# Kernel tuning notes

Measured on AMD Instinct MI355X. Metric: run time of the kernel, lower is better.

Reference implementation:

```python
import jax, jax.numpy as jnp
import numpy as np
from functools import partial

D = 256        # encoder_output_size
F = 256        # duration_predictor_filter_size
K = 3          # kernel size, padding=1
EPS = 1e-5
ALPHA = 1.0


def _xavier(key, shape, fan_in, fan_out, gain):
    a = gain * np.sqrt(6.0 / (fan_in + fan_out))
    return jax.random.uniform(key, shape, jnp.float32, -a, a)


def setup_inputs() -> dict:
    key = jax.random.key(0)
    ks = jax.random.split(key, 8)
    B, S = 32, 1024
    relu_gain = float(np.sqrt(2.0))
    inp = {
        "encoder_output": jax.random.normal(ks[0], (B, S, D), jnp.float32),
        "encoder_output_mask": jnp.ones((B, S, 1), jnp.float32),
        "target": jax.random.randint(ks[1], (B, S), 0, 3, jnp.int64),
        "mel_max_length": 4096,
        # conv weights in WIO layout [K, in, out]
        "W1": _xavier(ks[2], (K, D, F), D * K, F * K, relu_gain),
        "b1": jnp.zeros((F,), jnp.float32),
        "g1": jnp.ones((F,), jnp.float32),
        "beta1": jnp.zeros((F,), jnp.float32),
        "W2": _xavier(ks[3], (K, F, F), F * K, F * K, relu_gain),
        "b2": jnp.zeros((F,), jnp.float32),
        "g2": jnp.ones((F,), jnp.float32),
        "beta2": jnp.zeros((F,), jnp.float32),
        "Wl": _xavier(ks[4], (F, 1), F, 1, relu_gain),
        "bl": jnp.zeros((1,), jnp.float32),
    }
    return inp


def _conv1d(x, W, b):
    # x: [B,S,C], W: [K,Cin,Cout], padding=1 (same for K=3)
    y = jax.lax.conv_general_dilated(
        x, W, window_strides=(1,), padding=[(1, 1)],
        dimension_numbers=("NWC", "WIO", "NWC"))
    return y + b


def _layer_norm(x, g, b):
    mu = jnp.mean(x, axis=-1, keepdims=True)
    var = jnp.mean(jnp.square(x - mu), axis=-1, keepdims=True)
    return (x - mu) * jax.lax.rsqrt(var + EPS) * g + b


def _duration_predictor(x, mask, W1, b1, g1, beta1, W2, b2, g2, beta2, Wl, bl):
    x = x * mask
    h = jax.nn.relu(_layer_norm(_conv1d(x, W1, b1), g1, beta1))
    h = jax.nn.relu(_layer_norm(_conv1d(h, W2, b2), g2, beta2))
    d = jnp.einsum("bsf,fo->bso", h, Wl) + bl            # [B,S,1]
    d = jax.nn.relu(d * mask[:, :, 0:1])
    return d[..., 0]                                      # [B,S]


def _length_regulate(enc, target, alpha, mel_max_length):
    B, S, _ = enc.shape
    Tmax = mel_max_length
    # round-half-up as in the original rounding(), then +1 (source expands dur+1 times)
    reps = jnp.floor(target.astype(jnp.float32) * alpha + 0.5).astype(jnp.int32) + 1
    cum = jnp.cumsum(reps, axis=1)                        # [B,S]
    t = jnp.arange(Tmax, dtype=jnp.int32)                 # [Tmax]
    idx = jax.vmap(lambda c: jnp.searchsorted(c, t, side="right"))(cum)  # [B,Tmax]
    valid = t[None, :] < cum[:, -1:]                      # [B,Tmax]
    idx = jnp.minimum(idx, S - 1)
    out = jnp.take_along_axis(enc, idx[..., None], axis=1) * valid[..., None].astype(enc.dtype)
    pos = jnp.where(valid, t[None, :] + 1, 0).astype(jnp.int64)
    return out, pos


def reference(encoder_output, encoder_output_mask, target, mel_max_length,
              W1, b1, g1, beta1, W2, b2, g2, beta2, Wl, bl):
    dur_pred = _duration_predictor(encoder_output, encoder_output_mask,
                                   W1, b1, g1, beta1, W2, b2, g2, beta2, Wl, bl)
    output, decoder_pos = _length_regulate(encoder_output, target, ALPHA, mel_max_length)
    return output, decoder_pos, dur_pred
```

## Files before the change

### kernel.cpp

```cpp
#include <hip/hip_runtime.h>
#include <hip/hip_bf16.h>

#define BATCH 32
#define SEQ   1024
#define DCH   256
#define TMAX  4096
#define MROWS (BATCH * SEQ)
#define EPS   1e-5f

typedef __attribute__((ext_vector_type(8))) short s16x8;
typedef __attribute__((ext_vector_type(4))) float f32x4;

#define NSTEPS 24
#define WP_SHORTS (NSTEPS * 8192)

#define XROWS      68
#define H1_OFF     4096
#define H1_STRIDE  528
#define P_STRIDE   136
#define HP_STRIDE  68
#define ST_OFF     38944
#define LDS_TOTAL  39472

#define CONV_BLOCKS 512
#define REG_BLOCKS  2048
#define GRID_TOTAL  (CONV_BLOCKS + REG_BLOCKS)

__device__ __forceinline__ short f2bf_t(float f) {
    union { float f; unsigned u; } x; x.f = f;
    return (short)(x.u >> 16);
}
__device__ __forceinline__ short f2bf(float f) {
    union { float f; unsigned u; } x; x.f = f;
    unsigned r = x.u + 0x7fffu + ((x.u >> 16) & 1u);
    return (short)(r >> 16);
}
__device__ __forceinline__ unsigned pack_bf2(float lo, float hi) {
    union { float f; unsigned u; } a, b; a.f = lo; b.f = hi;
    return (a.u >> 16) | (b.u & 0xffff0000u);
}

__global__ __launch_bounds__(256) void prep_kernel(
    const float* __restrict__ W1, const float* __restrict__ W2,
    short* __restrict__ Wp1, short* __restrict__ Wp2,
    const int* __restrict__ target, int* __restrict__ idx,
    float* __restrict__ out_pos)
{
    const int bx  = blockIdx.x;
    const int tid = threadIdx.x;
    if (bx < 48) {
        const int s = bx % NSTEPS;
        const float* W = (bx < NSTEPS) ? W1 : W2;
        short* out = (bx < NSTEPS) ? Wp1 : Wp2;
        const int n  = tid;
        const int wv = n >> 6;
        const int nc = (n >> 4) & 3;
        const int cl = n & 15;
        const int ko = s >> 3;
        const int cb = (s & 7) * 32;
        #pragma unroll
        for (int q = 0; q < 4; ++q) {
            short v[8];
            #pragma unroll
            for (int j = 0; j < 8; ++j)
                v[j] = f2bf(W[(size_t)(ko * 256 + cb + q * 8 + j) * 256 + n]);
            short* dst = out + s * 8192 + wv * 2048 + nc * 512 + (q * 16 + cl) * 8;
            *(s16x8*)dst = *(const s16x8*)v;
        }
    } else {
        const int b = bx - 48;
        const int base = tid * 4;
        int reps[4], vals[4];
        int s = 0;
        #pragma unroll
        for (int j = 0; j < 4; ++j) {
            reps[j] = target[b * SEQ + base + j] + 1;
            s += reps[j];
            vals[j] = s;
        }
        const int lane = tid & 63;
        int tot = s;
        #pragma unroll
        for (int off = 1; off < 64; off <<= 1) {
            int t = __shfl_up(tot, off, 64);
            if (lane >= off) tot += t;
        }
        __shared__ int wsum[4];
        const int wid = tid >> 6;
        if (lane == 63) wsum[wid] = tot;
        __syncthreads();
        int woff = 0;
        for (int w = 0; w < wid; ++w) woff += wsum[w];
        const int total = wsum[0] + wsum[1] + wsum[2] + wsum[3];
        const int thr_excl = tot - s + woff;
        int* ib = idx + b * TMAX;
        #pragma unroll
        for (int j = 0; j < 4; ++j) {
            const int end   = thr_excl + vals[j];
            const int start = end - reps[j];
            for (int t = start; t < end; ++t) ib[t] = base + j;
        }
        for (int t = total + tid; t < TMAX; t += 256) ib[t] = -1;
        float* pb_ = out_pos + b * TMAX;
        for (int t = tid; t < TMAX; t += 256)
            pb_[t] = (t < total) ? (float)(t + 1) : 0.f;
    }
}

__global__ __launch_bounds__(256, 3) void fused_kernel(
    const float* __restrict__ enc,
    const float* __restrict__ mask,
    const short* __restrict__ Wp1,
    const short* __restrict__ Wp2,
    const float* __restrict__ cb1, const float* __restrict__ g1, const float* __restrict__ be1,
    const float* __restrict__ cb2, const float* __restrict__ g2, const float* __restrict__ be2,
    const float* __restrict__ Wl, const float* __restrict__ bl,
    float* __restrict__ out_dur,
    const int*  __restrict__ idx,
    float* __restrict__ out_main)
{
    __shared__ __align__(16) char lds[LDS_TOTAL];
    const int tid = threadIdx.x;
    const int bx  = blockIdx.x;

    if (bx >= CONV_BLOCKS) {
        const int r  = bx - CONV_BLOCKS;
        const int b  = r >> 6;
        const int t0 = (r & 63) * 64;
        int* sidx = (int*)lds;
        if (tid < 64) sidx[tid] = idx[b * TMAX + t0 + tid];
        __syncthreads();
        const int f4 = (tid & 63) * 4;
        const int rg = tid >> 6;
        #pragma unroll
        for (int g = 0; g < 16; ++g) {
            const int tt = g * 4 + rg;
            const int si = sidx[tt];
            float4 v = make_float4(0.f, 0.f, 0.f, 0.f);
            if (si >= 0)
                v = *reinterpret_cast<const float4*>(enc + (size_t)(b * SEQ + si) * 256 + f4);
            *reinterpret_cast<float4*>(out_main + (size_t)(b * TMAX + t0 + tt) * 256 + f4) = v;
        }
        return;
    }

    char* const Xst = lds;

    const int lane = tid & 63;
    const int wv   = tid >> 6;
    const int cl   = lane & 15;
    const int q    = lane >> 4;
    const int m0   = bx * 64;
    const int blo  = m0 & ~(SEQ - 1);
    const int bhi  = blo + SEQ;

    for (int t = tid; t < XROWS * 32; t += 256) {
        const int r  = t >> 5;
        const int ch = t & 31;
        const int grow = m0 - 2 + r;
        s16x8 v = {0, 0, 0, 0, 0, 0, 0, 0};
        if (grow >= blo && grow < bhi) {
            const float* xf = enc + (size_t)grow * DCH + ch * 8;
            const float4 f0 = *(const float4*)xf;
            const float4 f1 = *(const float4*)(xf + 4);
            const float mk = mask[grow];
            v[0] = f2bf_t(f0.x * mk); v[1] = f2bf_t(f0.y * mk);
            v[2] = f2bf_t(f0.z * mk); v[3] = f2bf_t(f0.w * mk);
            v[4] = f2bf_t(f1.x * mk); v[5] = f2bf_t(f1.y * mk);
            v[6] = f2bf_t(f1.z * mk); v[7] = f2bf_t(f1.w * mk);
        }
        *(s16x8*)(Xst + r * 512 + ((ch ^ (r & 7)) << 4)) = v;
    }

    f32x4 acc1[5][4];
    #pragma unroll
    for (int nc = 0; nc < 4; ++nc) {
        const f32x4 b4 = *(const f32x4*)(cb1 + wv * 64 + nc * 16 + q * 4);
        #pragma unroll
        for (int mr = 0; mr < 5; ++mr) acc1[mr][nc] = b4;
    }

    const short* wb1 = Wp1 + wv * 2048 + lane * 8;
    const short* wb2 = Wp2 + wv * 2048 + lane * 8;

#define G1_STEP(P, S)                                                         \
    {                                                                         \
        const int ko_  = (S) >> 3;                                            \
        const int chb_ = ((S) & 7) * 4 + q;                                   \
        _Pragma("unroll")                                                     \
        for (int mr = 0; mr < 5; ++mr) {                                      \
            int tr = mr * 16 + cl + ko_;                                      \
            if (mr == 4) tr = (tr < XROWS - 1) ? tr : (XROWS - 1);            \
            const s16x8 a = *(const s16x8*)(Xst + tr * 512 +                  \
                                            ((chb_ ^ (tr & 7)) << 4));        \
            _Pragma("unroll")                                                 \
            for (int nc = 0; nc < 4; ++nc)                                    \
                acc1[mr][nc] = __builtin_amdgcn_mfma_f32_16x16x32_bf16(       \
                    P[nc], a, acc1[mr][nc], 0, 0, 0);                         \
        }                                                                     \
    }
#define G2_STEP(P, S)                                                         \
    {                                                                         \
        const int ko_  = (S) >> 3;                                            \
        const int chb_ = ((S) & 7) * 4 + q;                                   \
        _Pragma("unroll")                                                     \
        for (int mr = 0; mr < 4; ++mr) {                                      \
            const int tr = mr * 16 + cl + ko_;                                \
            const s16x8 a = *(const s16x8*)(lds + H1_OFF + tr * H1_STRIDE +   \
                                            chb_ * 16);                       \
            _Pragma("unroll")                                                 \
            for (int nc = 0; nc < 4; ++nc)                                    \
                acc2[mr][nc] = __builtin_amdgcn_mfma_f32_16x16x32_bf16(       \
                    P[nc], a, acc2[mr][nc], 0, 0, 0);                         \
        }                                                                     \
    }
#define RELOAD(P, WB, S)                                                      \
    {                                                                         \
        const short* w_ = (WB) + (S) * 8192;                                  \
        _Pragma("unroll")                                                     \
        for (int nc = 0; nc < 4; ++nc)                                        \
            P[nc] = *(const s16x8*)(w_ + nc * 512);                           \
    }

    s16x8 pa[4], pb[4], pc[4];
    RELOAD(pa, wb1, 0)
    RELOAD(pb, wb1, 1)
    RELOAD(pc, wb1, 2)

    __syncthreads();

    for (int it = 0; it < 7; ++it) {
        const int s = it * 3;
        G1_STEP(pa, s)     RELOAD(pa, wb1, s + 3)
        G1_STEP(pb, s + 1) RELOAD(pb, wb1, s + 4)
        G1_STEP(pc, s + 2) RELOAD(pc, wb1, s + 5)
    }
    G1_STEP(pa, 21)
    G1_STEP(pb, 22)
    G1_STEP(pc, 23)

    float* st1 = (float*)(lds + ST_OFF);
    __syncthreads();
    #pragma unroll
    for (int mr = 0; mr < 5; ++mr) {
        float s1 = 0.f, s2 = 0.f;
        #pragma unroll
        for (int nc = 0; nc < 4; ++nc)
            #pragma unroll
            for (int rg = 0; rg < 4; ++rg) {
                const float v = acc1[mr][nc][rg];
                s1 += v; s2 += v * v;
            }
        const int hr = mr * 16 + cl;
        if (hr < 66)
            *(float2*)(lds + hr * P_STRIDE + (wv * 4 + q) * 8) = make_float2(s1, s2);
    }
    __syncthreads();
    if (tid < 66) {
        float s1 = 0.f, s2 = 0.f;
        #pragma unroll
        for (int k = 0; k < 16; ++k) {
            const int sl = (tid + k) & 15;
            const float2 v = *(const float2*)(lds + tid * P_STRIDE + sl * 8);
            s1 += v.x; s2 += v.y;
        }
        const float mean = s1 * (1.f / 256.f);
        const float var  = s2 * (1.f / 256.f) - mean * mean;
        st1[tid * 2]     = mean;
        st1[tid * 2 + 1] = rsqrtf(var + EPS);
    }
    __syncthreads();

    {
        #pragma unroll
        for (int mr = 0; mr < 5; ++mr) {
            const int hr = mr * 16 + cl;
            if (hr < 66) {
                const int grow = m0 - 1 + hr;
                const bool inb = (grow >= blo) && (grow < bhi);
                const float2 ms = *(const float2*)(st1 + hr * 2);
                #pragma unroll
                for (int nc = 0; nc < 4; ++nc) {
                    const int ch0 = wv * 64 + nc * 16 + q * 4;
                    const f32x4 g4 = *(const f32x4*)(g1 + ch0);
                    const f32x4 b4 = *(const f32x4*)(be1 + ch0);
                    float v[4];
                    #pragma unroll
                    for (int rg = 0; rg < 4; ++rg) {
                        float x = (acc1[mr][nc][rg] - ms.x) * ms.y * g4[rg] + b4[rg];
                        v[rg] = inb ? fmaxf(x, 0.f) : 0.f;
                    }
                    uint2 w;
                    w.x = pack_bf2(v[0], v[1]);
                    w.y = pack_bf2(v[2], v[3]);
                    *(uint2*)(lds + H1_OFF + hr * H1_STRIDE + ch0 * 2) = w;
                }
            }
        }
    }
    f32x4 acc2[4][4];
    RELOAD(pa, wb2, 0)
    RELOAD(pb, wb2, 1)
    RELOAD(pc, wb2, 2)
    #pragma unroll
    for (int nc = 0; nc < 4; ++nc) {
        const f32x4 b4 = *(const f32x4*)(cb2 + wv * 64 + nc * 16 + q * 4);
        #pragma unroll
        for (int mr = 0; mr < 4; ++mr) acc2[mr][nc] = b4;
    }
    __syncthreads();

    for (int it = 0; it < 7; ++it) {
        const int s = it * 3;
        G2_STEP(pa, s)     RELOAD(pa, wb2, s + 3)
        G2_STEP(pb, s + 1) RELOAD(pb, wb2, s + 4)
        G2_STEP(pc, s + 2) RELOAD(pc, wb2, s + 5)
    }
    G2_STEP(pa, 21)
    G2_STEP(pb, 22)
    G2_STEP(pc, 23)

    float* st2 = (float*)(lds + ST_OFF);
    __syncthreads();
    #pragma unroll
    for (int mr = 0; mr < 4; ++mr) {
        float s1 = 0.f, s2 = 0.f;
        #pragma unroll
        for (int nc = 0; nc < 4; ++nc)
            #pragma unroll
            for (int rg = 0; rg < 4; ++rg) {
                const float v = acc2[mr][nc][rg];
                s1 += v; s2 += v * v;
            }
        const int r = mr * 16 + cl;
        *(float2*)(lds + r * P_STRIDE + (wv * 4 + q) * 8) = make_float2(s1, s2);
    }
    __syncthreads();
    if (tid < 64) {
        float s1 = 0.f, s2 = 0.f;
        #pragma unroll
        for (int k = 0; k < 16; ++k) {
            const int sl = (tid + k) & 15;
            const float2 v = *(const float2*)(lds + tid * P_STRIDE + sl * 8);
            s1 += v.x; s2 += v.y;
        }
        const float mean = s1 * (1.f / 256.f);
        const float var  = s2 * (1.f / 256.f) - mean * mean;
        st2[tid * 2]     = mean;
        st2[tid * 2 + 1] = rsqrtf(var + EPS);
    }
    __syncthreads();

    {
        #pragma unroll
        for (int mr = 0; mr < 4; ++mr) {
            const int r = mr * 16 + cl;
            const float2 ms = *(const float2*)(st2 + r * 2);
            float p = 0.f;
            #pragma unroll
            for (int nc = 0; nc < 4; ++nc) {
                const int ch0 = wv * 64 + nc * 16 + q * 4;
                const f32x4 g4 = *(const f32x4*)(g2 + ch0);
                const f32x4 b4 = *(const f32x4*)(be2 + ch0);
                const f32x4 w4 = *(const f32x4*)(Wl + ch0);
                #pragma unroll
                for (int rg = 0; rg < 4; ++rg) {
                    float x = (acc2[mr][nc][rg] - ms.x) * ms.y * g4[rg] + b4[rg];
                    p += fmaxf(x, 0.f) * w4[rg];
                }
            }
            *(float*)(lds + r * HP_STRIDE + (wv * 4 + q) * 4) = p;
        }
        __syncthreads();
        if (tid < 64) {
            float d = 0.f;
            #pragma unroll
            for (int k = 0; k < 16; ++k) {
                const int sl = (tid + k) & 15;
                d += *(const float*)(lds + tid * HP_STRIDE + sl * 4);
            }
            d += bl[0];
            d *= mask[m0 + tid];
            out_dur[m0 + tid] = fmaxf(d, 0.f);
        }
    }
}

extern "C" void kernel_launch(void* const* d_in, const int* in_sizes, int n_in,
                              void* d_out, int out_size, void* d_ws, size_t ws_size,
                              hipStream_t stream) {
    const float* enc   = (const float*)d_in[0];
    const float* mask  = (const float*)d_in[1];
    const int*   target= (const int*)  d_in[2];
    const float* W1    = (const float*)d_in[4];
    const float* b1    = (const float*)d_in[5];
    const float* g1    = (const float*)d_in[6];
    const float* beta1 = (const float*)d_in[7];
    const float* W2    = (const float*)d_in[8];
    const float* b2    = (const float*)d_in[9];
    const float* g2    = (const float*)d_in[10];
    const float* beta2 = (const float*)d_in[11];
    const float* Wl    = (const float*)d_in[12];
    const float* bl    = (const float*)d_in[13];

    float* outF = (float*)d_out;
    float* out_main = outF;
    float* out_pos  = outF + (size_t)BATCH * TMAX * DCH;
    float* out_dur  = out_pos + (size_t)BATCH * TMAX;

    char* ws = (char*)d_ws;
    short* Wp1 = (short*)ws;
    short* Wp2 = Wp1 + WP_SHORTS;
    int*   idx = (int*)(Wp2 + WP_SHORTS);

    prep_kernel<<<80, 256, 0, stream>>>(W1, W2, Wp1, Wp2, target, idx, out_pos);
    fused_kernel<<<GRID_TOTAL, 256, 0, stream>>>(
        enc, mask, Wp1, Wp2,
        b1, g1, beta1, b2, g2, beta2, Wl, bl,
        out_dur, idx, out_main);
}
```

Measured before the change: 58.72 us.

## Split conv1 into two row passes and reuse input LDS for hidden activations

Conv1 accumulators are split into two passes (3 then 2 row tiles) so fewer accumulator registers are live at once, and the weight prefetch drops from triple to double buffering. The conv1 pre-norm output is stored as bf16 in place of the input tile, then LayerNorm+ReLU runs over LDS in a separate pass, which removes the separate H1 buffer and shrinks LDS. Cross-lane partial sums now use shuffles instead of 16-way LDS reductions. The cost is recomputing the weight stream twice for conv1, an extra LDS pass, and LN statistics taken from fp32 but applied to bf16-rounded values.

```diff
diff --git a/kernel.cpp b/kernel.cpp
--- a/kernel.cpp
+++ b/kernel.cpp
@@ -15,12 +15,9 @@
 #define WP_SHORTS (NSTEPS * 8192)
 
 #define XROWS      68
-#define H1_OFF     4096
-#define H1_STRIDE  528
-#define P_STRIDE   136
-#define HP_STRIDE  68
-#define ST_OFF     38944
-#define LDS_TOTAL  39472
+#define ST_OFF     34816
+#define PART_OFF   35344
+#define LDS_TOTAL  37984
 
 #define CONV_BLOCKS 512
 #define REG_BLOCKS  2048
@@ -38,6 +35,11 @@
 __device__ __forceinline__ unsigned pack_bf2(float lo, float hi) {
     union { float f; unsigned u; } a, b; a.f = lo; b.f = hi;
     return (a.u >> 16) | (b.u & 0xffff0000u);
+}
+__device__ __forceinline__ float bf2f(short s) {
+    union { unsigned u; float f; } x;
+    x.u = ((unsigned)(unsigned short)s) << 16;
+    return x.f;
 }
 
 __global__ __launch_bounds__(256) void prep_kernel(
@@ -107,6 +109,14 @@
     }
 }
 
+#define RELOAD(P, WB, S)                                                      \
+    {                                                                         \
+        const short* w_ = (WB) + (S) * 8192;                                  \
+        _Pragma("unroll")                                                     \
+        for (int nc = 0; nc < 4; ++nc)                                        \
+            P[nc] = *(const s16x8*)(w_ + nc * 512);                           \
+    }
+
 __global__ __launch_bounds__(256, 3) void fused_kernel(
     const float* __restrict__ enc,
     const float* __restrict__ mask,
@@ -172,158 +182,217 @@
         *(s16x8*)(Xst + r * 512 + ((ch ^ (r & 7)) << 4)) = v;
     }
 
-    f32x4 acc1[5][4];
+    const short* wb1 = Wp1 + wv * 2048 + lane * 8;
+    const short* wb2 = Wp2 + wv * 2048 + lane * 8;
+    float* st1 = (float*)(lds + ST_OFF);
+
+    s16x8 p0[4], p1[4];
+    RELOAD(p0, wb1, 0)
+    RELOAD(p1, wb1, 1)
+
+    f32x4 accA[3][4];
     #pragma unroll
     for (int nc = 0; nc < 4; ++nc) {
         const f32x4 b4 = *(const f32x4*)(cb1 + wv * 64 + nc * 16 + q * 4);
         #pragma unroll
-        for (int mr = 0; mr < 5; ++mr) acc1[mr][nc] = b4;
-    }
-
-    const short* wb1 = Wp1 + wv * 2048 + lane * 8;
-    const short* wb2 = Wp2 + wv * 2048 + lane * 8;
-
-#define G1_STEP(P, S)                                                         \
+        for (int mr = 0; mr < 3; ++mr) accA[mr][nc] = b4;
+    }
+    __syncthreads();
+
+#define GA_STEP(P, S)                                                         \
     {                                                                         \
         const int ko_  = (S) >> 3;                                            \
         const int chb_ = ((S) & 7) * 4 + q;                                   \
         _Pragma("unroll")                                                     \
-        for (int mr = 0; mr < 5; ++mr) {                                      \
-            int tr = mr * 16 + cl + ko_;                                      \
-            if (mr == 4) tr = (tr < XROWS - 1) ? tr : (XROWS - 1);            \
+        for (int mr = 0; mr < 3; ++mr) {                                      \
+            const int tr = mr * 16 + cl + ko_;                     \
             const s16x8 a = *(const s16x8*)(Xst + tr * 512 +                  \
                                             ((chb_ ^ (tr & 7)) << 4));        \
             _Pragma("unroll")                                                 \
             for (int nc = 0; nc < 4; ++nc)                                    \
-                acc1[mr][nc] = __builtin_amdgcn_mfma_f32_16x16x32_bf16(       \
-                    P[nc], a, acc1[mr][nc], 0, 0, 0);                         \
+                accA[mr][nc] = __builtin_amdgcn_mfma_f32_16x16x32_bf16(       \
+                    P[nc], a, accA[mr][nc], 0, 0, 0);                         \
         }                                                                     \
     }
+    for (int s = 0; s < NSTEPS; s += 2) {
+        GA_STEP(p0, s)
+        if (s + 2 < NSTEPS) RELOAD(p0, wb1, s + 2)
+        GA_STEP(p1, s + 1)
+        if (s + 3 < NSTEPS) RELOAD(p1, wb1, s + 3)
+    }
+
+    __syncthreads();
+
+    #pragma unroll
+    for (int mr = 0; mr < 3; ++mr) {
+        const int hr = mr * 16 + cl;
+        float s1 = 0.f, s2 = 0.f;
+        #pragma unroll
+        for (int nc = 0; nc < 4; ++nc)
+            #pragma unroll
+            for (int rg = 0; rg < 4; ++rg) {
+                const float v = accA[mr][nc][rg];
+                s1 += v; s2 += v * v;
+            }
+        s1 += __shfl_xor(s1, 16, 64); s1 += __shfl_xor(s1, 32, 64);
+        s2 += __shfl_xor(s2, 16, 64); s2 += __shfl_xor(s2, 32, 64);
+        if (lane < 16)
+            *(float2*)(lds + PART_OFF + hr * 40 + wv * 8) = make_float2(s1, s2);
+        #pragma unroll
+        for (int nc = 0; nc < 4; ++nc) {
+            const int ch0 = wv * 64 + nc * 16 + q * 4;
+            const int c16 = ch0 >> 3;
+            uint2 w;
+            w.x = pack_bf2(accA[mr][nc][0], accA[mr][nc][1]);
+            w.y = pack_bf2(accA[mr][nc][2], accA[mr][nc][3]);
+            *(uint2*)(lds + hr * 512 + ((c16 ^ (hr & 7)) << 4) + (q & 1) * 8) = w;
+        }
+    }
+
+    RELOAD(p0, wb1, 0)
+    RELOAD(p1, wb1, 1)
+    f32x4 accB[2][4];
+    #pragma unroll
+    for (int nc = 0; nc < 4; ++nc) {
+        const f32x4 b4 = *(const f32x4*)(cb1 + wv * 64 + nc * 16 + q * 4);
+        #pragma unroll
+        for (int mr = 0; mr < 2; ++mr) accB[mr][nc] = b4;
+    }
+#define GB_STEP(P, S)                                                         \
+    {                                                                         \
+        const int ko_  = (S) >> 3;                                            \
+        const int chb_ = ((S) & 7) * 4 + q;                                   \
+        _Pragma("unroll")                                                     \
+        for (int mr = 0; mr < 2; ++mr) {                                      \
+            int tr = 48 + mr * 16 + cl + ko_;                                 \
+            if (mr == 1) tr = (tr < XROWS - 1) ? tr : (XROWS - 1);            \
+            const s16x8 a = *(const s16x8*)(Xst + tr * 512 +                  \
+                                            ((chb_ ^ (tr & 7)) << 4));        \
+            _Pragma("unroll")                                                 \
+            for (int nc = 0; nc < 4; ++nc)                                    \
+                accB[mr][nc] = __builtin_amdgcn_mfma_f32_16x16x32_bf16(       \
+                    P[nc], a, accB[mr][nc], 0, 0, 0);                         \
+        }                                                                     \
+    }
+    for (int s = 0; s < NSTEPS; s += 2) {
+        GB_STEP(p0, s)
+        if (s + 2 < NSTEPS) RELOAD(p0, wb1, s + 2)
+        GB_STEP(p1, s + 1)
+        if (s + 3 < NSTEPS) RELOAD(p1, wb1, s + 3)
+    }
+
+    __syncthreads();
+
+    #pragma unroll
+    for (int mr = 0; mr < 2; ++mr) {
+        const int hr = 48 + mr * 16 + cl;
+        float s1 = 0.f, s2 = 0.f;
+        #pragma unroll
+        for (int nc = 0; nc < 4; ++nc)
+            #pragma unroll
+            for (int rg = 0; rg < 4; ++rg) {
+                const float v = accB[mr][nc][rg];
+                s1 += v; s2 += v * v;
+            }
+        s1 += __shfl_xor(s1, 16, 64); s1 += __shfl_xor(s1, 32, 64);
+        s2 += __shfl_xor(s2, 16, 64); s2 += __shfl_xor(s2, 32, 64);
+        if (hr < 66) {
+            if (lane < 16)
+                *(float2*)(lds + PART_OFF + hr * 40 + wv * 8) = make_float2(s1, s2);
+            #pragma unroll
+            for (int nc = 0; nc < 4; ++nc) {
+                const int ch0 = wv * 64 + nc * 16 + q * 4;
+                const int c16 = ch0 >> 3;
+                uint2 w;
+                w.x = pack_bf2(accB[mr][nc][0], accB[mr][nc][1]);
+                w.y = pack_bf2(accB[mr][nc][2], accB[mr][nc][3]);
+                *(uint2*)(lds + hr * 512 + ((c16 ^ (hr & 7)) << 4) + (q & 1) * 8) = w;
+            }
+        }
+    }
+
+    RELOAD(p0, wb2, 0)
+    RELOAD(p1, wb2, 1)
+
+    __syncthreads();
+
+    if (tid < 66) {
+        const char* pb = lds + PART_OFF + tid * 40;
+        const float2 a0 = *(const float2*)pb;
+        const float2 a1 = *(const float2*)(pb + 8);
+        const float2 a2 = *(const float2*)(pb + 16);
+        const float2 a3 = *(const float2*)(pb + 24);
+        const float s1 = a0.x + a1.x + a2.x + a3.x;
+        const float s2 = a0.y + a1.y + a2.y + a3.y;
+        const float mean = s1 * (1.f / 256.f);
+        const float var  = s2 * (1.f / 256.f) - mean * mean;
+        st1[tid * 2]     = mean;
+        st1[tid * 2 + 1] = rsqrtf(var + EPS);
+    }
+    __syncthreads();
+
+    for (int i = tid; i < 66 * 32; i += 256) {
+        const int r   = i >> 5;
+        const int c16 = i & 31;
+        char* p = lds + r * 512 + ((c16 ^ (r & 7)) << 4);
+        const int grow = m0 - 1 + r;
+        if (grow >= blo && grow < bhi) {
+            const float2 ms = *(const float2*)(st1 + r * 2);
+            const f32x4 gA = *(const f32x4*)(g1 + c16 * 8);
+            const f32x4 gB = *(const f32x4*)(g1 + c16 * 8 + 4);
+            const f32x4 bA = *(const f32x4*)(be1 + c16 * 8);
+            const f32x4 bB = *(const f32x4*)(be1 + c16 * 8 + 4);
+            s16x8 v = *(s16x8*)p;
+            s16x8 o;
+            #pragma unroll
+            for (int j = 0; j < 8; ++j) {
+                const float x  = bf2f(v[j]);
+                const float gg = (j < 4) ? gA[j] : gB[j - 4];
+                const float bb = (j < 4) ? bA[j] : bB[j - 4];
+                const float y  = (x - ms.x) * ms.y * gg + bb;
+                o[j] = f2bf_t(fmaxf(y, 0.f));
+            }
+            *(s16x8*)p = o;
+        } else {
+            s16x8 z = {0, 0, 0, 0, 0, 0, 0, 0};
+            *(s16x8*)p = z;
+        }
+    }
+
+    f32x4 acc2[4][4];
+    #pragma unroll
+    for (int nc = 0; nc < 4; ++nc) {
+        const f32x4 b4 = *(const f32x4*)(cb2 + wv * 64 + nc * 16 + q * 4);
+        #pragma unroll
+        for (int mr = 0; mr < 4; ++mr) acc2[mr][nc] = b4;
+    }
+    __syncthreads();
+
 #define G2_STEP(P, S)                                                         \
     {                                                                         \
         const int ko_  = (S) >> 3;                                            \
         const int chb_ = ((S) & 7) * 4 + q;                                   \
         _Pragma("unroll")                                                     \
         for (int mr = 0; mr < 4; ++mr) {                                      \
-            const int tr = mr * 16 + cl + ko_;                                \
-            const s16x8 a = *(const s16x8*)(lds + H1_OFF + tr * H1_STRIDE +   \
-                                            chb_ * 16);                       \
+            const int tr = mr * 16 + cl + ko_;                     \
+            const s16x8 a = *(const s16x8*)(Xst + tr * 512 +                  \
+                                            ((chb_ ^ (tr & 7)) << 4));        \
             _Pragma("unroll")                                                 \
             for (int nc = 0; nc < 4; ++nc)                                    \
                 acc2[mr][nc] = __builtin_amdgcn_mfma_f32_16x16x32_bf16(       \
                     P[nc], a, acc2[mr][nc], 0, 0, 0);                         \
         }                                                                     \
     }
-#define RELOAD(P, WB, S)                                                      \
-    {                                                                         \
-        const short* w_ = (WB) + (S) * 8192;                                  \
-        _Pragma("unroll")                                                     \
-        for (int nc = 0; nc < 4; ++nc)                                        \
-            P[nc] = *(const s16x8*)(w_ + nc * 512);                           \
-    }
-
-    s16x8 pa[4], pb[4], pc[4];
-    RELOAD(pa, wb1, 0)
-    RELOAD(pb, wb1, 1)
-    RELOAD(pc, wb1, 2)
-
-    __syncthreads();
-
-    for (int it = 0; it < 7; ++it) {
-        const int s = it * 3;
-        G1_STEP(pa, s)     RELOAD(pa, wb1, s + 3)
-        G1_STEP(pb, s + 1) RELOAD(pb, wb1, s + 4)
-        G1_STEP(pc, s + 2) RELOAD(pc, wb1, s + 5)
-    }
-    G1_STEP(pa, 21)
-    G1_STEP(pb, 22)
-    G1_STEP(pc, 23)
-
-    float* st1 = (float*)(lds + ST_OFF);
-    __syncthreads();
-    #pragma unroll
-    for (int mr = 0; mr < 5; ++mr) {
-        float s1 = 0.f, s2 = 0.f;
-        #pragma unroll
-        for (int nc = 0; nc < 4; ++nc)
-            #pragma unroll
-            for (int rg = 0; rg < 4; ++rg) {
-                const float v = acc1[mr][nc][rg];
-                s1 += v; s2 += v * v;
-            }
-        const int hr = mr * 16 + cl;
-        if (hr < 66)
-            *(float2*)(lds + hr * P_STRIDE + (wv * 4 + q) * 8) = make_float2(s1, s2);
-    }
-    __syncthreads();
-    if (tid < 66) {
-        float s1 = 0.f, s2 = 0.f;
-        #pragma unroll
-        for (int k = 0; k < 16; ++k) {
-            const int sl = (tid + k) & 15;
-            const float2 v = *(const float2*)(lds + tid * P_STRIDE + sl * 8);
-            s1 += v.x; s2 += v.y;
-        }
-        const float mean = s1 * (1.f / 256.f);
-        const float var  = s2 * (1.f / 256.f) - mean * mean;
-        st1[tid * 2]     = mean;
-        st1[tid * 2 + 1] = rsqrtf(var + EPS);
-    }
-    __syncthreads();
-
-    {
-        #pragma unroll
-        for (int mr = 0; mr < 5; ++mr) {
-            const int hr = mr * 16 + cl;
-            if (hr < 66) {
-                const int grow = m0 - 1 + hr;
-                const bool inb = (grow >= blo) && (grow < bhi);
-                const float2 ms = *(const float2*)(st1 + hr * 2);
-                #pragma unroll
-                for (int nc = 0; nc < 4; ++nc) {
-                    const int ch0 = wv * 64 + nc * 16 + q * 4;
-                    const f32x4 g4 = *(const f32x4*)(g1 + ch0);
-                    const f32x4 b4 = *(const f32x4*)(be1 + ch0);
-                    float v[4];
-                    #pragma unroll
-                    for (int rg = 0; rg < 4; ++rg) {
-                        float x = (acc1[mr][nc][rg] - ms.x) * ms.y * g4[rg] + b4[rg];
-                        v[rg] = inb ? fmaxf(x, 0.f) : 0.f;
-                    }
-                    uint2 w;
-                    w.x = pack_bf2(v[0], v[1]);
-                    w.y = pack_bf2(v[2], v[3]);
-                    *(uint2*)(lds + H1_OFF + hr * H1_STRIDE + ch0 * 2) = w;
-                }
-            }
-        }
-    }
-    f32x4 acc2[4][4];
-    RELOAD(pa, wb2, 0)
-    RELOAD(pb, wb2, 1)
-    RELOAD(pc, wb2, 2)
-    #pragma unroll
-    for (int nc = 0; nc < 4; ++nc) {
-        const f32x4 b4 = *(const f32x4*)(cb2 + wv * 64 + nc * 16 + q * 4);
-        #pragma unroll
-        for (int mr = 0; mr < 4; ++mr) acc2[mr][nc] = b4;
-    }
-    __syncthreads();
-
-    for (int it = 0; it < 7; ++it) {
-        const int s = it * 3;
-        G2_STEP(pa, s)     RELOAD(pa, wb2, s + 3)
-        G2_STEP(pb, s + 1) RELOAD(pb, wb2, s + 4)
-        G2_STEP(pc, s + 2) RELOAD(pc, wb2, s + 5)
-    }
-    G2_STEP(pa, 21)
-    G2_STEP(pb, 22)
-    G2_STEP(pc, 23)
-
-    float* st2 = (float*)(lds + ST_OFF);
-    __syncthreads();
+    for (int s = 0; s < NSTEPS; s += 2) {
+        G2_STEP(p0, s)
+        if (s + 2 < NSTEPS) RELOAD(p0, wb2, s + 2)
+        G2_STEP(p1, s + 1)
+        if (s + 3 < NSTEPS) RELOAD(p1, wb2, s + 3)
+    }
+
     #pragma unroll
     for (int mr = 0; mr < 4; ++mr) {
+        const int r = mr * 16 + cl;
         float s1 = 0.f, s2 = 0.f;
         #pragma unroll
         for (int nc = 0; nc < 4; ++nc)
@@ -332,18 +401,21 @@
                 const float v = acc2[mr][nc][rg];
                 s1 += v; s2 += v * v;
             }
-        const int r = mr * 16 + cl;
-        *(float2*)(lds + r * P_STRIDE + (wv * 4 + q) * 8) = make_float2(s1, s2);
-    }
-    __syncthreads();
+        s1 += __shfl_xor(s1, 16, 64); s1 += __shfl_xor(s1, 32, 64);
+        s2 += __shfl_xor(s2, 16, 64); s2 += __shfl_xor(s2, 32, 64);
+        if (lane < 16)
+            *(float2*)(lds + PART_OFF + r * 40 + wv * 8) = make_float2(s1, s2);
+    }
+    __syncthreads();
+    float* st2 = st1;
     if (tid < 64) {
-        float s1 = 0.f, s2 = 0.f;
-        #pragma unroll
-        for (int k = 0; k < 16; ++k) {
-            const int sl = (tid + k) & 15;
-            const float2 v = *(const float2*)(lds + tid * P_STRIDE + sl * 8);
-            s1 += v.x; s2 += v.y;
-        }
+        const char* pb = lds + PART_OFF + tid * 40;
+        const float2 a0 = *(const float2*)pb;
+        const float2 a1 = *(const float2*)(pb + 8);
+        const float2 a2 = *(const float2*)(pb + 16);
+        const float2 a3 = *(const float2*)(pb + 24);
+        const float s1 = a0.x + a1.x + a2.x + a3.x;
+        const float s2 = a0.y + a1.y + a2.y + a3.y;
         const float mean = s1 * (1.f / 256.f);
         const float var  = s2 * (1.f / 256.f) - mean * mean;
         st2[tid * 2]     = mean;
@@ -351,38 +423,33 @@
     }
     __syncthreads();
 
-    {
-        #pragma unroll
-        for (int mr = 0; mr < 4; ++mr) {
-            const int r = mr * 16 + cl;
-            const float2 ms = *(const float2*)(st2 + r * 2);
-            float p = 0.f;
-            #pragma unroll
-            for (int nc = 0; nc < 4; ++nc) {
-                const int ch0 = wv * 64 + nc * 16 + q * 4;
-                const f32x4 g4 = *(const f32x4*)(g2 + ch0);
-                const f32x4 b4 = *(const f32x4*)(be2 + ch0);
-                const f32x4 w4 = *(const f32x4*)(Wl + ch0);
-                #pragma unroll
-                for (int rg = 0; rg < 4; ++rg) {
-                    float x = (acc2[mr][nc][rg] - ms.x) * ms.y * g4[rg] + b4[rg];
-                    p += fmaxf(x, 0.f) * w4[rg];
-                }
-            }
-            *(float*)(lds + r * HP_STRIDE + (wv * 4 + q) * 4) = p;
-        }
-        __syncthreads();
-        if (tid < 64) {
-            float d = 0.f;
-            #pragma unroll
-            for (int k = 0; k < 16; ++k) {
-                const int sl = (tid + k) & 15;
-                d += *(const float*)(lds + tid * HP_STRIDE + sl * 4);
-            }
-            d += bl[0];
-            d *= mask[m0 + tid];
-            out_dur[m0 + tid] = fmaxf(d, 0.f);
-        }
+    #pragma unroll
+    for (int mr = 0; mr < 4; ++mr) {
+        const int r = mr * 16 + cl;
+        const float2 ms = *(const float2*)(st2 + r * 2);
+        float p = 0.f;
+        #pragma unroll
+        for (int nc = 0; nc < 4; ++nc) {
+            const int ch0 = wv * 64 + nc * 16 + q * 4;
+            const f32x4 g4 = *(const f32x4*)(g2 + ch0);
+            const f32x4 b4 = *(const f32x4*)(be2 + ch0);
+            const f32x4 w4 = *(const f32x4*)(Wl + ch0);
+            #pragma unroll
+            for (int rg = 0; rg < 4; ++rg) {
+                const float x = (acc2[mr][nc][rg] - ms.x) * ms.y * g4[rg] + b4[rg];
+                p += fmaxf(x, 0.f) * w4[rg];
+            }
+        }
+        p += __shfl_xor(p, 16, 64); p += __shfl_xor(p, 32, 64);
+        if (lane < 16)
+            *(float*)(lds + PART_OFF + r * 20 + wv * 4) = p;
+    }
+    __syncthreads();
+    if (tid < 64) {
+        const f32x4 v = *(const f32x4*)(lds + PART_OFF + tid * 20);
+        float d = (v[0] + v[1]) + (v[2] + v[3]) + bl[0];
+        d *= mask[m0 + tid];
+        out_dur[m0 + tid] = fmaxf(d, 0.f);
     }
 }
 
```

After: 85.30 us. +45.3%, slower.
